# Performance work log

Measured on AMD Instinct MI355X. Metric: run time of the kernel, lower is better.

## Reference

```python
import jax, jax.numpy as jnp
import numpy as np

B, L, D = 1, 2048, 512
NL, N, K = 4, 16, 4
DI = 2 * D          # mamba expand=2
R = D // 16         # dt_rank = ceil(D/16)
H = 4 * D           # mlp hidden


def _ln(x, w, b, eps=1e-5):
    mu = x.mean(-1, keepdims=True)
    v = ((x - mu) ** 2).mean(-1, keepdims=True)
    return (x - mu) * jax.lax.rsqrt(v + eps) * w + b


def _rms(x, w, eps=1e-5):
    return x * jax.lax.rsqrt((x * x).mean(-1, keepdims=True) + eps) * w


def _ssm_scan(delta, Bm, Cm, u, A, Dp):
    # delta,u: (B,L,DI); Bm,Cm: (B,L,N); A: (DI,N); Dp: (DI,)
    def step(h, inp):
        d_t, b_t, c_t, u_t = inp                              # (B,DI),(B,N),(B,N),(B,DI)
        dA = jnp.exp(d_t[..., None] * A)                      # (B,DI,N)
        h = dA * h + (d_t * u_t)[..., None] * b_t[:, None, :]
        y = jnp.einsum('bdn,bn->bd', h, c_t)
        return h, y
    h0 = jnp.zeros((delta.shape[0], DI, N), delta.dtype)
    xs = (delta.swapaxes(0, 1), Bm.swapaxes(0, 1), Cm.swapaxes(0, 1), u.swapaxes(0, 1))
    _, ys = jax.lax.scan(step, h0, xs)
    return ys.swapaxes(0, 1) + u * Dp


def _mamba(h, in_w, cw, cb, xw, dtw, dtb, A_log, Dp, ow):
    xz = h @ in_w.T                                           # (B,L,2*DI)
    x, z = jnp.split(xz, 2, axis=-1)
    # causal depthwise conv1d, kernel K, left pad K-1
    xp = jnp.pad(x, ((0, 0), (K - 1, 0), (0, 0)))
    Ls = x.shape[1]
    x = sum(cw[:, k] * xp[:, k:k + Ls, :] for k in range(K)) + cb
    x = jax.nn.silu(x)
    dbc = x @ xw.T                                            # (B,L,R+2N)
    dt, Bm, Cm = dbc[..., :R], dbc[..., R:R + N], dbc[..., R + N:]
    delta = jax.nn.softplus(dt @ dtw.T + dtb)                 # (B,L,DI)
    A = -jnp.exp(A_log)                                       # (DI,N)
    y = _ssm_scan(delta, Bm, Cm, x, A, Dp)
    y = y * jax.nn.silu(z)
    return y @ ow.T


def _forward(hidden_states, ln1_w, ln1_b, in_proj_w, conv_w, conv_b, x_proj_w,
             dt_proj_w, dt_proj_b, A_log, D_param, out_proj_w, block_norm_w,
             norm_f_w, ln2_w, ln2_b, fc1_w, fc1_b, fc2_w, fc2_b):
    shortcut = hidden_states
    h = _ln(hidden_states, ln1_w, ln1_b)
    residual = None
    for i in range(in_proj_w.shape[0]):
        residual = h if residual is None else h + residual    # residual_in_fp32
        hn = _rms(residual, block_norm_w[i])                  # fused_add_norm prenorm
        h = _mamba(hn, in_proj_w[i], conv_w[i], conv_b[i], x_proj_w[i],
                   dt_proj_w[i], dt_proj_b[i], A_log[i], D_param[i], out_proj_w[i])
    h = _rms(h + residual, norm_f_w)                          # final rms_norm_fn
    h = shortcut + h
    x = _ln(h, ln2_w, ln2_b)
    x = jax.nn.gelu(x @ fc1_w.T + fc1_b)
    x = x @ fc2_w.T + fc2_b
    return h + x


def setup_inputs() -> dict:
    key = jax.random.key(0)
    ks = jax.random.split(key, 9)
    s = 0.02
    return {
        'hidden_states': jax.random.normal(ks[0], (B, L, D), jnp.float32),
        'ln1_w': jnp.ones((D,), jnp.float32),
        'ln1_b': jnp.zeros((D,), jnp.float32),
        'in_proj_w': jax.random.normal(ks[1], (NL, 2 * DI, D), jnp.float32) * s,
        'conv_w': jax.random.normal(ks[2], (NL, DI, K), jnp.float32) * 0.3,
        'conv_b': jnp.zeros((NL, DI), jnp.float32),
        'x_proj_w': jax.random.normal(ks[3], (NL, R + 2 * N, DI), jnp.float32) * s,
        'dt_proj_w': jax.random.normal(ks[4], (NL, DI, R), jnp.float32) * s,
        'dt_proj_b': jax.random.uniform(ks[5], (NL, DI), jnp.float32, -4.0, -2.0),
        'A_log': jnp.tile(jnp.log(jnp.arange(1, N + 1, dtype=jnp.float32)), (NL, DI, 1)),
        'D_param': jnp.ones((NL, DI), jnp.float32),
        'out_proj_w': jax.random.normal(ks[6], (NL, D, DI), jnp.float32) * s,
        'block_norm_w': jnp.ones((NL, D), jnp.float32),
        'norm_f_w': jnp.ones((D,), jnp.float32),
        'ln2_w': jnp.ones((D,), jnp.float32),
        'ln2_b': jnp.zeros((D,), jnp.float32),
        'fc1_w': jax.random.normal(ks[7], (H, D), jnp.float32) * s,
        'fc1_b': jnp.zeros((H,), jnp.float32),
        'fc2_w': jax.random.normal(ks[8], (D, H), jnp.float32) * s,
        'fc2_b': jnp.zeros((D,), jnp.float32),
    }


def reference(hidden_states, ln1_w, ln1_b, in_proj_w, conv_w, conv_b, x_proj_w,
              dt_proj_w, dt_proj_b, A_log, D_param, out_proj_w, block_norm_w,
              norm_f_w, ln2_w, ln2_b, fc1_w, fc1_b, fc2_w, fc2_b):
    return _forward(hidden_states, ln1_w, ln1_b, in_proj_w, conv_w, conv_b,
                    x_proj_w, dt_proj_w, dt_proj_b, A_log, D_param, out_proj_w,
                    block_norm_w, norm_f_w, ln2_w, ln2_b, fc1_w, fc1_b, fc2_w, fc2_b)
```

## Files before the change

kernel.cpp:

```cpp
#include <hip/hip_runtime.h>
#include <hip/hip_bf16.h>
#include <math.h>

#define L_SEQ 2048
#define Dm    512
#define DI    1024
#define Nst   16
#define Kc    4
#define Rr    32
#define NL    4
#define CH    128
#define LC    (L_SEQ / CH)
#define KSX   8

typedef __attribute__((ext_vector_type(8))) short bf16x8;
typedef __attribute__((ext_vector_type(4))) float f32x4;

__device__ __forceinline__ float act_softplus(float x) {
    return fmaxf(x, 0.f) + log1pf(__expf(-fabsf(x)));
}
__device__ __forceinline__ float act_gelu(float x) {
    float c = 0.7978845608028654f * (x + 0.044715f * x * x * x);
    float t = 1.f - 2.f / (__expf(2.f * c) + 1.f);
    return 0.5f * x * (1.f + t);
}
__device__ __forceinline__ float silu_(float x) {
    return x / (1.f + __expf(-x));
}
__device__ __forceinline__ ushort f2bf(float f) {
    union { float f; unsigned u; } c; c.f = f;
    unsigned r = c.u + 0x7fffu + ((c.u >> 16) & 1u);
    return (ushort)(r >> 16);
}
__device__ __forceinline__ float bf2f(ushort u) {
    union { unsigned u; float f; } c; c.u = ((unsigned)u) << 16;
    return c.f;
}
__device__ __forceinline__ float wave_sum(float v) {
    #pragma unroll
    for (int off = 32; off; off >>= 1) v += __shfl_xor(v, off);
    return v;
}

__global__ __launch_bounds__(256) void cast_all_kernel(
    const float* __restrict__ s0, ushort* __restrict__ d0, int n0,
    const float* __restrict__ s1, ushort* __restrict__ d1, int n1,
    const float* __restrict__ s2, ushort* __restrict__ d2, int n2,
    const float* __restrict__ s3, ushort* __restrict__ d3, int n3,
    const float* __restrict__ s4, ushort* __restrict__ d4, int n4_,
    const float* __restrict__ s5, ushort* __restrict__ d5, int n5)
{
    int i = blockIdx.x * 256 + threadIdx.x;
    const float* s; ushort* d;
    if (i < n0) { s = s0; d = d0; }
    else { i -= n0; if (i < n1) { s = s1; d = d1; }
    else { i -= n1; if (i < n2) { s = s2; d = d2; }
    else { i -= n2; if (i < n3) { s = s3; d = d3; }
    else { i -= n3; if (i < n4_) { s = s4; d = d4; }
    else { i -= n4_; if (i < n5) { s = s5; d = d5; } else return; } } } } }
    float4 v = ((const float4*)s)[i];
    ushort4 o;
    o.x = f2bf(v.x); o.y = f2bf(v.y); o.z = f2bf(v.z); o.w = f2bf(v.w);
    ((ushort4*)d)[i] = o;
}

__global__ __launch_bounds__(256) void ln_rms_kernel(const float* __restrict__ x,
    const float* __restrict__ w, const float* __restrict__ b,
    const float* __restrict__ rw, float* __restrict__ res,
    ushort* __restrict__ hn_bf)
{
    int lane = threadIdx.x & 63, wv = threadIdx.x >> 6;
    int row = blockIdx.x * 4 + wv;
    size_t base = (size_t)row * Dm + lane * 8;
    float v[8];
    *(float4*)(v)     = *(const float4*)(x + base);
    *(float4*)(v + 4) = *(const float4*)(x + base + 4);
    float s = 0.f, ss = 0.f;
    #pragma unroll
    for (int q = 0; q < 8; ++q) { s += v[q]; ss += v[q] * v[q]; }
    s = wave_sum(s); ss = wave_sum(ss);
    float mu = s * (1.f / Dm);
    float rs = rsqrtf(ss * (1.f / Dm) - mu * mu + 1e-5f);
    float wv8[8], bv8[8], rv8[8];
    *(float4*)(wv8)     = *(const float4*)(w + lane * 8);
    *(float4*)(wv8 + 4) = *(const float4*)(w + lane * 8 + 4);
    *(float4*)(bv8)     = *(const float4*)(b + lane * 8);
    *(float4*)(bv8 + 4) = *(const float4*)(b + lane * 8 + 4);
    *(float4*)(rv8)     = *(const float4*)(rw + lane * 8);
    *(float4*)(rv8 + 4) = *(const float4*)(rw + lane * 8 + 4);
    float o[8], ss2 = 0.f;
    #pragma unroll
    for (int q = 0; q < 8; ++q) {
        o[q] = (v[q] - mu) * rs * wv8[q] + bv8[q];
        ss2 += o[q] * o[q];
    }
    *(float4*)(res + base)     = *(float4*)(o);
    *(float4*)(res + base + 4) = *(float4*)(o + 4);
    ss2 = wave_sum(ss2);
    float rr = rsqrtf(ss2 * (1.f / Dm) + 1e-5f);
    bf16x8 hb;
    #pragma unroll
    for (int q = 0; q < 8; ++q) hb[q] = (short)f2bf(o[q] * rr * rv8[q]);
    *(bf16x8*)(hn_bf + base) = hb;
}

__global__ __launch_bounds__(256) void add_rms_kernel(const ushort* __restrict__ hb,
    float* __restrict__ res, const float* __restrict__ w, ushort* __restrict__ rms_out)
{
    int lane = threadIdx.x & 63, wv = threadIdx.x >> 6;
    int row = blockIdx.x * 4 + wv;
    size_t base = (size_t)row * Dm + lane * 8;
    bf16x8 hv = *(const bf16x8*)(hb + base);
    float v[8];
    *(float4*)(v)     = *(const float4*)(res + base);
    *(float4*)(v + 4) = *(const float4*)(res + base + 4);
    float ss = 0.f;
    #pragma unroll
    for (int q = 0; q < 8; ++q) {
        v[q] += bf2f((ushort)hv[q]);
        ss += v[q] * v[q];
    }
    *(float4*)(res + base)     = *(float4*)(v);
    *(float4*)(res + base + 4) = *(float4*)(v + 4);
    ss = wave_sum(ss);
    float rr = rsqrtf(ss * (1.f / Dm) + 1e-5f);
    float wv8[8];
    *(float4*)(wv8)     = *(const float4*)(w + lane * 8);
    *(float4*)(wv8 + 4) = *(const float4*)(w + lane * 8 + 4);
    bf16x8 ob;
    #pragma unroll
    for (int q = 0; q < 8; ++q) ob[q] = (short)f2bf(v[q] * rr * wv8[q]);
    *(bf16x8*)(rms_out + base) = ob;
}

__global__ __launch_bounds__(256) void final_ln2_kernel(const ushort* __restrict__ hb,
    const float* __restrict__ res, const float* __restrict__ shortcut,
    const float* __restrict__ wf, const float* __restrict__ w2,
    const float* __restrict__ b2, float* __restrict__ hout,
    ushort* __restrict__ yb16)
{
    int lane = threadIdx.x & 63, wv = threadIdx.x >> 6;
    int row = blockIdx.x * 4 + wv;
    size_t base = (size_t)row * Dm + lane * 8;
    bf16x8 hv = *(const bf16x8*)(hb + base);
    float v[8];
    *(float4*)(v)     = *(const float4*)(res + base);
    *(float4*)(v + 4) = *(const float4*)(res + base + 4);
    float ss = 0.f;
    #pragma unroll
    for (int q = 0; q < 8; ++q) {
        v[q] += bf2f((ushort)hv[q]);
        ss += v[q] * v[q];
    }
    ss = wave_sum(ss);
    float rs = rsqrtf(ss * (1.f / Dm) + 1e-5f);
    float sc[8], wf8[8];
    *(float4*)(sc)     = *(const float4*)(shortcut + base);
    *(float4*)(sc + 4) = *(const float4*)(shortcut + base + 4);
    *(float4*)(wf8)     = *(const float4*)(wf + lane * 8);
    *(float4*)(wf8 + 4) = *(const float4*)(wf + lane * 8 + 4);
    float t[8], s2 = 0.f, ss2 = 0.f;
    #pragma unroll
    for (int q = 0; q < 8; ++q) {
        t[q] = sc[q] + v[q] * rs * wf8[q];
        s2 += t[q]; ss2 += t[q] * t[q];
    }
    *(float4*)(hout + base)     = *(float4*)(t);
    *(float4*)(hout + base + 4) = *(float4*)(t + 4);
    s2 = wave_sum(s2); ss2 = wave_sum(ss2);
    float mu = s2 * (1.f / Dm);
    float rsig = rsqrtf(ss2 * (1.f / Dm) - mu * mu + 1e-5f);
    float w28[8], b28[8];
    *(float4*)(w28)     = *(const float4*)(w2 + lane * 8);
    *(float4*)(w28 + 4) = *(const float4*)(w2 + lane * 8 + 4);
    *(float4*)(b28)     = *(const float4*)(b2 + lane * 8);
    *(float4*)(b28 + 4) = *(const float4*)(b2 + lane * 8 + 4);
    bf16x8 ob;
    #pragma unroll
    for (int q = 0; q < 8; ++q) ob[q] = (short)f2bf((t[q] - mu) * rsig * w28[q] + b28[q]);
    *(bf16x8*)(yb16 + base) = ob;
}

template<int BM, int BN, int BK, int EPI, int KS = 1>
__global__ __launch_bounds__(256) void gemm_mfma(
    const ushort* __restrict__ A, int lda,
    const ushort* __restrict__ W, int K,
    void* __restrict__ Cout, int ldc,
    const float* __restrict__ bias, const float* __restrict__ addsrc,
    size_t split_stride)
{
    constexpr int ROWB  = BK * 2;
    constexpr int SMASK = (ROWB / 16) - 1;
    constexpr int KK    = BK / 32;
    constexpr int WM = BM / 2, WN = BN / 2;
    constexpr int FM = WM / 16, FN = WN / 16;
    constexpr int ISS_A = (BM * ROWB) / 4096;
    constexpr int ISS_W = (BN * ROWB) / 4096;

    __shared__ __align__(16) ushort As[BM * BK];
    __shared__ __align__(16) ushort Ws[BN * BK];

    int tid = threadIdx.x;
    int wave = tid >> 6, lane = tid & 63;
    int wr = wave >> 1, wc = wave & 1;
    int l16 = lane & 15, lk = lane >> 4;
    int bm = blockIdx.y * BM, bn = blockIdx.x * BN;

    int kbeg = 0, kend = K;
    float* coutf = (float*)Cout;
    if constexpr (KS > 1) {
        int Kper = K / KS;
        kbeg = blockIdx.z * Kper; kend = kbeg + Kper;
        coutf += split_stride * blockIdx.z;
    }

    const ushort* srcA[ISS_A];
    const ushort* srcW[ISS_W];
    #pragma unroll
    for (int s = 0; s < ISS_A; ++s) {
        int off = s * 4096 + wave * 1024 + lane * 16;
        int row = off / ROWB;
        int slot = (off % ROWB) >> 4;
        int col = ((slot ^ (row & SMASK)) << 3);
        srcA[s] = A + (size_t)(bm + row) * lda + col;
    }
    #pragma unroll
    for (int s = 0; s < ISS_W; ++s) {
        int off = s * 4096 + wave * 1024 + lane * 16;
        int row = off / ROWB;
        int slot = (off % ROWB) >> 4;
        int col = ((slot ^ (row & SMASK)) << 3);
        srcW[s] = W + (size_t)(bn + row) * K + col;
    }
    int aoff[FM][KK], woff[FN][KK];
    #pragma unroll
    for (int i = 0; i < FM; ++i) {
        int row = wr * WM + i * 16 + l16;
        #pragma unroll
        for (int kk = 0; kk < KK; ++kk)
            aoff[i][kk] = row * BK + ((((kk << 2) | lk) ^ (row & SMASK)) << 3);
    }
    #pragma unroll
    for (int j = 0; j < FN; ++j) {
        int row = wc * WN + j * 16 + l16;
        #pragma unroll
        for (int kk = 0; kk < KK; ++kk)
            woff[j][kk] = row * BK + ((((kk << 2) | lk) ^ (row & SMASK)) << 3);
    }

    f32x4 acc[FM][FN] = {};

    for (int k0 = kbeg; k0 < kend; k0 += BK) {
        #pragma unroll
        for (int s = 0; s < ISS_A; ++s)
            __builtin_amdgcn_global_load_lds(
                (const __attribute__((address_space(1))) void*)(srcA[s] + k0),
                (__attribute__((address_space(3))) void*)((char*)As + s * 4096 + wave * 1024),
                16, 0, 0);
        #pragma unroll
        for (int s = 0; s < ISS_W; ++s)
            __builtin_amdgcn_global_load_lds(
                (const __attribute__((address_space(1))) void*)(srcW[s] + k0),
                (__attribute__((address_space(3))) void*)((char*)Ws + s * 4096 + wave * 1024),
                16, 0, 0);
        __syncthreads();
        #pragma unroll
        for (int kk = 0; kk < KK; ++kk) {
            bf16x8 af[FM], wf[FN];
            #pragma unroll
            for (int i = 0; i < FM; ++i) af[i] = *(const bf16x8*)(As + aoff[i][kk]);
            #pragma unroll
            for (int j = 0; j < FN; ++j) wf[j] = *(const bf16x8*)(Ws + woff[j][kk]);
            #pragma unroll
            for (int i = 0; i < FM; ++i)
                #pragma unroll
                for (int j = 0; j < FN; ++j)
                    acc[i][j] = __builtin_amdgcn_mfma_f32_16x16x32_bf16(af[i], wf[j], acc[i][j], 0, 0, 0);
        }
        __syncthreads();
    }

    int orow0 = bm + wr * WM, ocol0 = bn + wc * WN;
    #pragma unroll
    for (int j = 0; j < FN; ++j) {
        int col = ocol0 + j * 16 + l16;
        float bj = 0.f;
        if constexpr (EPI == 2 || EPI == 4) bj = bias[col];
        #pragma unroll
        for (int i = 0; i < FM; ++i) {
            #pragma unroll
            for (int r = 0; r < 4; ++r) {
                int row = orow0 + i * 16 + lk * 4 + r;
                float v = acc[i][j][r];
                if constexpr (EPI == 0) {
                    coutf[(size_t)row * ldc + col] = v;
                } else if constexpr (EPI == 1) {
                    ((ushort*)Cout)[(size_t)row * ldc + col] = f2bf(v);
                } else if constexpr (EPI == 2) {
                    ((ushort*)Cout)[(size_t)row * ldc + col] = f2bf(act_gelu(v + bj));
                } else if constexpr (EPI == 4) {
                    ((float*)Cout)[(size_t)row * ldc + col] = v + bj + addsrc[(size_t)row * ldc + col];
                }
            }
        }
    }
}

__global__ __launch_bounds__(256) void conv_silu_kernel(const ushort* __restrict__ xz,
    const float* __restrict__ cw, const float* __restrict__ cb, ushort* __restrict__ xc)
{
    int g = blockIdx.x * 256 + threadIdx.x;
    int e = g * 8;
    int d0 = e & (DI - 1);
    int t = e >> 10;
    float acc[8];
    #pragma unroll
    for (int q = 0; q < 8; ++q) acc[q] = cb[d0 + q];
    float4 cwv[8];
    #pragma unroll
    for (int q = 0; q < 8; ++q) cwv[q] = *(const float4*)(cw + (size_t)(d0 + q) * 4);
    #pragma unroll
    for (int k = 0; k < 4; ++k) {
        int tt = t + k - 3;
        if (tt >= 0) {
            bf16x8 xv = *(const bf16x8*)(xz + (size_t)tt * (2 * DI) + d0);
            #pragma unroll
            for (int q = 0; q < 8; ++q) {
                float wk = (k == 0) ? cwv[q].x : (k == 1) ? cwv[q].y : (k == 2) ? cwv[q].z : cwv[q].w;
                acc[q] = fmaf(wk, bf2f((ushort)xv[q]), acc[q]);
            }
        }
    }
    bf16x8 o;
    #pragma unroll
    for (int q = 0; q < 8; ++q) o[q] = (short)f2bf(silu_(acc[q]));
    *(bf16x8*)(xc + e) = o;
}

__global__ __launch_bounds__(256) void scan_chunk_kernel(
    const float* __restrict__ part, const ushort* __restrict__ u,
    const ushort* __restrict__ wdt, const float* __restrict__ dtb,
    const float* __restrict__ A_log,
    float* __restrict__ hend, float* __restrict__ aprod,
    ushort* __restrict__ delta_bf)
{
    __shared__ float sdt[LC][32];
    __shared__ float bsm[LC][16];
    int tid = threadIdx.x;
    int c = blockIdx.x;
    int d = blockIdx.y * 256 + tid;
    int t0 = c * LC;
    const int S = L_SEQ * 64;
    for (int i = tid; i < LC * 48; i += 256) {
        int tt = i / 48, cc = i % 48;
        int idx = (t0 + tt) * 64 + cc;
        float s = 0.f;
        #pragma unroll
        for (int p = 0; p < KSX; ++p) s += part[idx + p * S];
        if (cc < 32) sdt[tt][cc] = s; else bsm[tt][cc - 32] = s;
    }
    bf16x8 wd[4];
    #pragma unroll
    for (int p = 0; p < 4; ++p) wd[p] = *(const bf16x8*)(wdt + (size_t)d * 32 + p * 8);
    float bd = dtb[d];
    float A2[16];
    {
        float a[16];
        #pragma unroll
        for (int q = 0; q < 4; ++q)
            *(float4*)(a + q * 4) = ((const float4*)(A_log + (size_t)d * 16))[q];
        #pragma unroll
        for (int n = 0; n < 16; ++n)
            A2[n] = -__expf(a[n]) * 1.44269504f;
    }
    float h[16], ap[16];
    #pragma unroll
    for (int n = 0; n < 16; ++n) { h[n] = 0.f; ap[n] = 1.f; }
    __syncthreads();
    for (int tt = 0; tt < LC; ++tt) {
        int t = t0 + tt;
        float dtv = bd;
        #pragma unroll
        for (int p = 0; p < 4; ++p)
            #pragma unroll
            for (int e = 0; e < 8; ++e)
                dtv = fmaf(sdt[tt][p * 8 + e], bf2f((ushort)wd[p][e]), dtv);
        ushort dbf = f2bf(act_softplus(dtv));
        delta_bf[(size_t)t * DI + d] = dbf;
        float dt_ = bf2f(dbf);
        float du = dt_ * bf2f(u[(size_t)t * DI + d]);
        #pragma unroll
        for (int n = 0; n < 16; ++n) {
            float dA = exp2f(dt_ * A2[n]);
            h[n] = fmaf(dA, h[n], du * bsm[tt][n]);
            ap[n] *= dA;
        }
    }
    size_t base = ((size_t)c * DI + d) * 16;
    #pragma unroll
    for (int q = 0; q < 4; ++q) {
        ((float4*)(hend + base))[q]  = *(float4*)(h + q * 4);
        ((float4*)(aprod + base))[q] = *(float4*)(ap + q * 4);
    }
}

__global__ __launch_bounds__(64) void chunk_prefix_kernel(
    const float* __restrict__ hend, float* __restrict__ aprod_hin)
{
    int j = blockIdx.x * 64 + threadIdx.x;
    float h = 0.f;
    for (int cg = 0; cg < CH; cg += 8) {
        float ap[8], he[8];
        #pragma unroll
        for (int q = 0; q < 8; ++q) {
            size_t o = (size_t)(cg + q) * (DI * Nst) + j;
            ap[q] = aprod_hin[o]; he[q] = hend[o];
        }
        #pragma unroll
        for (int q = 0; q < 8; ++q) {
            size_t o = (size_t)(cg + q) * (DI * Nst) + j;
            aprod_hin[o] = h;
            h = fmaf(ap[q], h, he[q]);
        }
    }
}

__global__ __launch_bounds__(256) void scan_apply_kernel(
    const float* __restrict__ part, const ushort* __restrict__ delta,
    const ushort* __restrict__ u, const float* __restrict__ A_log,
    const float* __restrict__ Dp, const ushort* __restrict__ xz,
    const float* __restrict__ hin, ushort* __restrict__ y)
{
    __shared__ float bsm[LC][16], csm[LC][16];
    int tid = threadIdx.x;
    int c = blockIdx.x;
    int d = blockIdx.y * 256 + tid;
    int t0 = c * LC;
    const int S = L_SEQ * 64;
    for (int i = tid; i < LC * 32; i += 256) {
        int tt = i >> 5, k = i & 31;
        int idx = (t0 + tt) * 64 + 32 + k;
        float s = 0.f;
        #pragma unroll
        for (int p = 0; p < KSX; ++p) s += part[idx + p * S];
        if (k < 16) bsm[tt][k] = s; else csm[tt][k - 16] = s;
    }
    float A2[16];
    {
        float a[16];
        #pragma unroll
        for (int q = 0; q < 4; ++q)
            *(float4*)(a + q * 4) = ((const float4*)(A_log + (size_t)d * 16))[q];
        #pragma unroll
        for (int n = 0; n < 16; ++n)
            A2[n] = -__expf(a[n]) * 1.44269504f;
    }
    float h[16];
    size_t base = ((size_t)c * DI + d) * 16;
    #pragma unroll
    for (int q = 0; q < 4; ++q)
        *(float4*)(h + q * 4) = ((const float4*)(hin + base))[q];
    float Dval = Dp[d];
    __syncthreads();
    for (int tt = 0; tt < LC; ++tt) {
        int t = t0 + tt;
        float dt_ = bf2f(delta[(size_t)t * DI + d]);
        float u_  = bf2f(u[(size_t)t * DI + d]);
        float du  = dt_ * u_;
        float acc = 0.f;
        #pragma unroll
        for (int n = 0; n < 16; ++n) {
            float dA = exp2f(dt_ * A2[n]);
            h[n] = fmaf(dA, h[n], du * bsm[tt][n]);
            acc = fmaf(h[n], csm[tt][n], acc);
        }
        float zv = bf2f(xz[(size_t)t * (2 * DI) + DI + d]);
        y[(size_t)t * DI + d] = f2bf((acc + u_ * Dval) * silu_(zv));
    }
}

extern "C" void kernel_launch(void* const* d_in, const int* in_sizes, int n_in,
                              void* d_out, int out_size, void* d_ws, size_t ws_size,
                              hipStream_t stream)
{
    const float* hidden     = (const float*)d_in[0];
    const float* ln1_w      = (const float*)d_in[1];
    const float* ln1_b      = (const float*)d_in[2];
    const float* in_proj_w  = (const float*)d_in[3];
    const float* conv_w     = (const float*)d_in[4];
    const float* conv_b     = (const float*)d_in[5];
    const float* x_proj_w   = (const float*)d_in[6];
    const float* dt_proj_w  = (const float*)d_in[7];
    const float* dt_proj_b  = (const float*)d_in[8];
    const float* A_log      = (const float*)d_in[9];
    const float* D_param    = (const float*)d_in[10];
    const float* out_proj_w = (const float*)d_in[11];
    const float* block_norm_w = (const float*)d_in[12];
    const float* norm_f_w   = (const float*)d_in[13];
    const float* ln2_w      = (const float*)d_in[14];
    const float* ln2_b      = (const float*)d_in[15];
    const float* fc1_w      = (const float*)d_in[16];
    const float* fc1_b      = (const float*)d_in[17];
    const float* fc2_w      = (const float*)d_in[18];
    const float* fc2_b      = (const float*)d_in[19];

    char* P = (char*)d_ws;
    auto alloc = [&](size_t bytes) { char* r = P; P += (bytes + 255) & ~(size_t)255; return r; };
    float* hout   = (float*)alloc((size_t)L_SEQ * Dm * 4);
    float* res    = (float*)alloc((size_t)L_SEQ * Dm * 4);
    float* part   = (float*)alloc((size_t)KSX * L_SEQ * 64 * 4);
    float* hend   = (float*)alloc((size_t)CH * DI * Nst * 4);
    float* aprod  = (float*)alloc((size_t)CH * DI * Nst * 4);
    ushort* h_bf  = (ushort*)alloc((size_t)L_SEQ * Dm * 2);
    ushort* delta_bf = (ushort*)alloc((size_t)L_SEQ * DI * 2);
    ushort* hn_bf = (ushort*)alloc((size_t)L_SEQ * Dm * 2);
    ushort* xz_bf = (ushort*)alloc((size_t)L_SEQ * 2 * DI * 2);
    ushort* xc_bf = (ushort*)alloc((size_t)L_SEQ * DI * 2);
    ushort* yb_bf = (ushort*)alloc((size_t)L_SEQ * DI * 2);
    ushort* w_in  = (ushort*)alloc((size_t)NL * 2 * DI * Dm * 2);
    ushort* w_out = (ushort*)alloc((size_t)NL * Dm * DI * 2);
    ushort* w_x   = (ushort*)alloc((size_t)NL * 64 * DI * 2);
    ushort* w_dt  = (ushort*)alloc((size_t)NL * DI * Rr * 2);
    ushort* w_fc1 = (ushort*)alloc((size_t)(4 * Dm) * Dm * 2);
    ushort* w_fc2 = (ushort*)alloc((size_t)Dm * (4 * Dm) * 2);
    float* out  = (float*)d_out;

    {
        int n0 = NL * 2 * DI * Dm / 4, n1 = NL * Dm * DI / 4, n2 = NL * 64 * DI / 4;
        int n3 = NL * DI * Rr / 4, n4_ = 4 * Dm * Dm / 4, n5 = Dm * 4 * Dm / 4;
        int tot = n0 + n1 + n2 + n3 + n4_ + n5;
        cast_all_kernel<<<(tot + 255) / 256, 256, 0, stream>>>(
            in_proj_w, w_in, n0, out_proj_w, w_out, n1, x_proj_w, w_x, n2,
            dt_proj_w, w_dt, n3, fc1_w, w_fc1, n4_, fc2_w, w_fc2, n5);
    }

    ln_rms_kernel<<<L_SEQ / 4, 256, 0, stream>>>(hidden, ln1_w, ln1_b,
                                                 block_norm_w, res, hn_bf);

    dim3 gscan(CH, DI / 256);
    for (int i = 0; i < NL; ++i) {
        if (i) add_rms_kernel<<<L_SEQ / 4, 256, 0, stream>>>(h_bf, res,
                                                  block_norm_w + i * Dm, hn_bf);
        gemm_mfma<128, 128, 128, 1><<<dim3(2 * DI / 128, L_SEQ / 128), 256, 0, stream>>>(
            hn_bf, Dm, w_in + (size_t)i * 2 * DI * Dm, Dm, xz_bf, 2 * DI, nullptr, nullptr, 0);
        conv_silu_kernel<<<(L_SEQ * DI / 8) / 256, 256, 0, stream>>>(
            xz_bf, conv_w + i * DI * Kc, conv_b + i * DI, xc_bf);
        gemm_mfma<64, 64, 64, 0, KSX><<<dim3(1, L_SEQ / 64, KSX), 256, 0, stream>>>(
            xc_bf, DI, w_x + (size_t)i * 64 * DI, DI, part, 64, nullptr, nullptr,
            (size_t)L_SEQ * 64);
        scan_chunk_kernel<<<gscan, 256, 0, stream>>>(part, xc_bf,
                                        w_dt + (size_t)i * DI * Rr, dt_proj_b + i * DI,
                                        A_log + (size_t)i * DI * Nst, hend, aprod, delta_bf);
        chunk_prefix_kernel<<<(DI * Nst) / 64, 64, 0, stream>>>(hend, aprod);
        scan_apply_kernel<<<gscan, 256, 0, stream>>>(part, delta_bf, xc_bf,
                                        A_log + (size_t)i * DI * Nst,
                                        D_param + i * DI, xz_bf, aprod, yb_bf);
        gemm_mfma<64, 64, 128, 1><<<dim3(Dm / 64, L_SEQ / 64), 256, 0, stream>>>(
            yb_bf, DI, w_out + (size_t)i * Dm * DI, DI, h_bf, Dm, nullptr, nullptr, 0);
    }

    final_ln2_kernel<<<L_SEQ / 4, 256, 0, stream>>>(h_bf, res, hidden, norm_f_w,
                                                ln2_w, ln2_b, hout, hn_bf);
    gemm_mfma<128, 128, 128, 2><<<dim3(2048 / 128, L_SEQ / 128), 256, 0, stream>>>(
        hn_bf, Dm, w_fc1, Dm, xz_bf, 2048, fc1_b, nullptr, 0);
    gemm_mfma<64, 64, 128, 4><<<dim3(Dm / 64, L_SEQ / 64), 256, 0, stream>>>(
        xz_bf, 2048, w_fc2, 2048, out, Dm, fc2_b, hout, 0);
}
```

Before: 429.5 us.

## Fuse chunked scan phases into one persistent kernel with grid barriers

Merges scan_chunk, chunk_prefix and scan_apply into a single 512-block kernel that synchronises through a hierarchical atomic grid barrier (8 groups of 64 blocks). The delta intermediate is no longer stored; dt is recomputed from shared memory in the second pass. The prefix phase now runs on 64 blocks of 256 threads instead of 256 blocks of 64. The initial LayerNorm/RMS kernel is folded into the weight-cast kernel, which also zeroes the barrier counters. This removes two launches per layer and the delta round trip. In exchange it adds barrier spin cost and depends on all 512 blocks being co-resident, with launch_bounds(256,2) as the occupancy hint.

Result: slower. 1.681 ms (+291.5%).

```diff
diff --git a/kernel.cpp b/kernel.cpp
--- a/kernel.cpp
+++ b/kernel.cpp
@@ -42,15 +42,82 @@
     return v;
 }
 
-__global__ __launch_bounds__(256) void cast_all_kernel(
+__device__ __forceinline__ void hbar(unsigned* base, int g, int grpSize, int nGrps) {
+    __syncthreads();
+    __threadfence();
+    if (threadIdx.x == 0) {
+        unsigned* grp  = base + g * 16;
+        unsigned* glob = base + 8 * 16;
+        unsigned* rel  = base + (9 + g) * 16;
+        unsigned prev = __hip_atomic_fetch_add(grp, 1u, __ATOMIC_ACQ_REL, __HIP_MEMORY_SCOPE_AGENT);
+        if (prev == (unsigned)(grpSize - 1)) {
+            __hip_atomic_fetch_add(glob, 1u, __ATOMIC_ACQ_REL, __HIP_MEMORY_SCOPE_AGENT);
+            while (__hip_atomic_load(glob, __ATOMIC_ACQUIRE, __HIP_MEMORY_SCOPE_AGENT) < (unsigned)nGrps)
+                __builtin_amdgcn_s_sleep(2);
+            __hip_atomic_store(rel, 1u, __ATOMIC_RELEASE, __HIP_MEMORY_SCOPE_AGENT);
+        } else {
+            while (__hip_atomic_load(rel, __ATOMIC_ACQUIRE, __HIP_MEMORY_SCOPE_AGENT) == 0u)
+                __builtin_amdgcn_s_sleep(2);
+        }
+    }
+    __syncthreads();
+    __threadfence();
+}
+
+__global__ __launch_bounds__(256) void setup_kernel(
     const float* __restrict__ s0, ushort* __restrict__ d0, int n0,
     const float* __restrict__ s1, ushort* __restrict__ d1, int n1,
     const float* __restrict__ s2, ushort* __restrict__ d2, int n2,
     const float* __restrict__ s3, ushort* __restrict__ d3, int n3,
     const float* __restrict__ s4, ushort* __restrict__ d4, int n4_,
-    const float* __restrict__ s5, ushort* __restrict__ d5, int n5)
-{
-    int i = blockIdx.x * 256 + threadIdx.x;
+    const float* __restrict__ s5, ushort* __restrict__ d5, int n5,
+    const float* __restrict__ x, const float* __restrict__ w,
+    const float* __restrict__ b, const float* __restrict__ rw,
+    float* __restrict__ res, ushort* __restrict__ hn_bf,
+    unsigned* __restrict__ ctr)
+{
+    if (blockIdx.x < 512) {
+        int lane = threadIdx.x & 63, wv = threadIdx.x >> 6;
+        int row = blockIdx.x * 4 + wv;
+        size_t base = (size_t)row * Dm + lane * 8;
+        float v[8];
+        *(float4*)(v)     = *(const float4*)(x + base);
+        *(float4*)(v + 4) = *(const float4*)(x + base + 4);
+        float s = 0.f, ss = 0.f;
+        #pragma unroll
+        for (int q = 0; q < 8; ++q) { s += v[q]; ss += v[q] * v[q]; }
+        s = wave_sum(s); ss = wave_sum(ss);
+        float mu = s * (1.f / Dm);
+        float rs = rsqrtf(ss * (1.f / Dm) - mu * mu + 1e-5f);
+        float wv8[8], bv8[8], rv8[8];
+        *(float4*)(wv8)     = *(const float4*)(w + lane * 8);
+        *(float4*)(wv8 + 4) = *(const float4*)(w + lane * 8 + 4);
+        *(float4*)(bv8)     = *(const float4*)(b + lane * 8);
+        *(float4*)(bv8 + 4) = *(const float4*)(b + lane * 8 + 4);
+        *(float4*)(rv8)     = *(const float4*)(rw + lane * 8);
+        *(float4*)(rv8 + 4) = *(const float4*)(rw + lane * 8 + 4);
+        float o[8], ss2 = 0.f;
+        #pragma unroll
+        for (int q = 0; q < 8; ++q) {
+            o[q] = (v[q] - mu) * rs * wv8[q] + bv8[q];
+            ss2 += o[q] * o[q];
+        }
+        *(float4*)(res + base)     = *(float4*)(o);
+        *(float4*)(res + base + 4) = *(float4*)(o + 4);
+        ss2 = wave_sum(ss2);
+        float rr = rsqrtf(ss2 * (1.f / Dm) + 1e-5f);
+        bf16x8 hb;
+        #pragma unroll
+        for (int q = 0; q < 8; ++q) hb[q] = (short)f2bf(o[q] * rr * rv8[q]);
+        *(bf16x8*)(hn_bf + base) = hb;
+        return;
+    }
+    int cb = blockIdx.x - 512;
+    if (cb == 0) {
+        #pragma unroll
+        for (int q = 0; q < 16; ++q) ctr[threadIdx.x * 16 + q] = 0u;
+    }
+    int i = cb * 256 + threadIdx.x;
     const float* s; ushort* d;
     if (i < n0) { s = s0; d = d0; }
     else { i -= n0; if (i < n1) { s = s1; d = d1; }
@@ -62,46 +129,6 @@
     ushort4 o;
     o.x = f2bf(v.x); o.y = f2bf(v.y); o.z = f2bf(v.z); o.w = f2bf(v.w);
     ((ushort4*)d)[i] = o;
-}
-
-__global__ __launch_bounds__(256) void ln_rms_kernel(const float* __restrict__ x,
-    const float* __restrict__ w, const float* __restrict__ b,
-    const float* __restrict__ rw, float* __restrict__ res,
-    ushort* __restrict__ hn_bf)
-{
-    int lane = threadIdx.x & 63, wv = threadIdx.x >> 6;
-    int row = blockIdx.x * 4 + wv;
-    size_t base = (size_t)row * Dm + lane * 8;
-    float v[8];
-    *(float4*)(v)     = *(const float4*)(x + base);
-    *(float4*)(v + 4) = *(const float4*)(x + base + 4);
-    float s = 0.f, ss = 0.f;
-    #pragma unroll
-    for (int q = 0; q < 8; ++q) { s += v[q]; ss += v[q] * v[q]; }
-    s = wave_sum(s); ss = wave_sum(ss);
-    float mu = s * (1.f / Dm);
-    float rs = rsqrtf(ss * (1.f / Dm) - mu * mu + 1e-5f);
-    float wv8[8], bv8[8], rv8[8];
-    *(float4*)(wv8)     = *(const float4*)(w + lane * 8);
-    *(float4*)(wv8 + 4) = *(const float4*)(w + lane * 8 + 4);
-    *(float4*)(bv8)     = *(const float4*)(b + lane * 8);
-    *(float4*)(bv8 + 4) = *(const float4*)(b + lane * 8 + 4);
-    *(float4*)(rv8)     = *(const float4*)(rw + lane * 8);
-    *(float4*)(rv8 + 4) = *(const float4*)(rw + lane * 8 + 4);
-    float o[8], ss2 = 0.f;
-    #pragma unroll
-    for (int q = 0; q < 8; ++q) {
-        o[q] = (v[q] - mu) * rs * wv8[q] + bv8[q];
-        ss2 += o[q] * o[q];
-    }
-    *(float4*)(res + base)     = *(float4*)(o);
-    *(float4*)(res + base + 4) = *(float4*)(o + 4);
-    ss2 = wave_sum(ss2);
-    float rr = rsqrtf(ss2 * (1.f / Dm) + 1e-5f);
-    bf16x8 hb;
-    #pragma unroll
-    for (int q = 0; q < 8; ++q) hb[q] = (short)f2bf(o[q] * rr * rv8[q]);
-    *(bf16x8*)(hn_bf + base) = hb;
 }
 
 __global__ __launch_bounds__(256) void add_rms_kernel(const ushort* __restrict__ hb,
@@ -337,27 +364,35 @@
     *(bf16x8*)(xc + e) = o;
 }
 
-__global__ __launch_bounds__(256) void scan_chunk_kernel(
+__global__ __launch_bounds__(256, 2) void scan_fused_kernel(
     const float* __restrict__ part, const ushort* __restrict__ u,
     const ushort* __restrict__ wdt, const float* __restrict__ dtb,
-    const float* __restrict__ A_log,
+    const float* __restrict__ A_log, const float* __restrict__ Dp,
+    const ushort* __restrict__ xz,
     float* __restrict__ hend, float* __restrict__ aprod,
-    ushort* __restrict__ delta_bf)
+    ushort* __restrict__ y, unsigned* __restrict__ ctr)
 {
     __shared__ float sdt[LC][32];
     __shared__ float bsm[LC][16];
+    __shared__ float csm[LC][16];
     int tid = threadIdx.x;
-    int c = blockIdx.x;
-    int d = blockIdx.y * 256 + tid;
+    int bid = blockIdx.x;
+    int c = bid & (CH - 1);
+    int yg = bid >> 7;
+    int d = yg * 256 + tid;
+    int g = bid & 7;
     int t0 = c * LC;
     const int S = L_SEQ * 64;
-    for (int i = tid; i < LC * 48; i += 256) {
-        int tt = i / 48, cc = i % 48;
+
+    for (int i = tid; i < LC * 64; i += 256) {
+        int tt = i >> 6, cc = i & 63;
         int idx = (t0 + tt) * 64 + cc;
         float s = 0.f;
         #pragma unroll
         for (int p = 0; p < KSX; ++p) s += part[idx + p * S];
-        if (cc < 32) sdt[tt][cc] = s; else bsm[tt][cc - 32] = s;
+        if (cc < 32) sdt[tt][cc] = s;
+        else if (cc < 48) bsm[tt][cc - 32] = s;
+        else csm[tt][cc - 48] = s;
     }
     bf16x8 wd[4];
     #pragma unroll
@@ -377,6 +412,7 @@
     #pragma unroll
     for (int n = 0; n < 16; ++n) { h[n] = 0.f; ap[n] = 1.f; }
     __syncthreads();
+
     for (int tt = 0; tt < LC; ++tt) {
         int t = t0 + tt;
         float dtv = bd;
@@ -385,92 +421,64 @@
             #pragma unroll
             for (int e = 0; e < 8; ++e)
                 dtv = fmaf(sdt[tt][p * 8 + e], bf2f((ushort)wd[p][e]), dtv);
-        ushort dbf = f2bf(act_softplus(dtv));
-        delta_bf[(size_t)t * DI + d] = dbf;
-        float dt_ = bf2f(dbf);
-        float du = dt_ * bf2f(u[(size_t)t * DI + d]);
+        dtv = act_softplus(dtv);
+        float du = dtv * bf2f(u[(size_t)t * DI + d]);
         #pragma unroll
         for (int n = 0; n < 16; ++n) {
-            float dA = exp2f(dt_ * A2[n]);
+            float dA = exp2f(dtv * A2[n]);
             h[n] = fmaf(dA, h[n], du * bsm[tt][n]);
             ap[n] *= dA;
         }
     }
-    size_t base = ((size_t)c * DI + d) * 16;
+    size_t sbase = ((size_t)c * DI + d) * 16;
     #pragma unroll
     for (int q = 0; q < 4; ++q) {
-        ((float4*)(hend + base))[q]  = *(float4*)(h + q * 4);
-        ((float4*)(aprod + base))[q] = *(float4*)(ap + q * 4);
-    }
-}
-
-__global__ __launch_bounds__(64) void chunk_prefix_kernel(
-    const float* __restrict__ hend, float* __restrict__ aprod_hin)
-{
-    int j = blockIdx.x * 64 + threadIdx.x;
-    float h = 0.f;
-    for (int cg = 0; cg < CH; cg += 8) {
-        float ap[8], he[8];
-        #pragma unroll
-        for (int q = 0; q < 8; ++q) {
-            size_t o = (size_t)(cg + q) * (DI * Nst) + j;
-            ap[q] = aprod_hin[o]; he[q] = hend[o];
-        }
-        #pragma unroll
-        for (int q = 0; q < 8; ++q) {
-            size_t o = (size_t)(cg + q) * (DI * Nst) + j;
-            aprod_hin[o] = h;
-            h = fmaf(ap[q], h, he[q]);
-        }
-    }
-}
-
-__global__ __launch_bounds__(256) void scan_apply_kernel(
-    const float* __restrict__ part, const ushort* __restrict__ delta,
-    const ushort* __restrict__ u, const float* __restrict__ A_log,
-    const float* __restrict__ Dp, const ushort* __restrict__ xz,
-    const float* __restrict__ hin, ushort* __restrict__ y)
-{
-    __shared__ float bsm[LC][16], csm[LC][16];
-    int tid = threadIdx.x;
-    int c = blockIdx.x;
-    int d = blockIdx.y * 256 + tid;
-    int t0 = c * LC;
-    const int S = L_SEQ * 64;
-    for (int i = tid; i < LC * 32; i += 256) {
-        int tt = i >> 5, k = i & 31;
-        int idx = (t0 + tt) * 64 + 32 + k;
-        float s = 0.f;
-        #pragma unroll
-        for (int p = 0; p < KSX; ++p) s += part[idx + p * S];
-        if (k < 16) bsm[tt][k] = s; else csm[tt][k - 16] = s;
-    }
-    float A2[16];
-    {
-        float a[16];
-        #pragma unroll
-        for (int q = 0; q < 4; ++q)
-            *(float4*)(a + q * 4) = ((const float4*)(A_log + (size_t)d * 16))[q];
-        #pragma unroll
-        for (int n = 0; n < 16; ++n)
-            A2[n] = -__expf(a[n]) * 1.44269504f;
-    }
-    float h[16];
-    size_t base = ((size_t)c * DI + d) * 16;
+        ((float4*)(hend + sbase))[q]  = *(float4*)(h + q * 4);
+        ((float4*)(aprod + sbase))[q] = *(float4*)(ap + q * 4);
+    }
+
+    hbar(ctr, g, 64, 8);
+
+    if (bid < 64) {
+        int j = bid * 256 + tid;
+        float hh = 0.f;
+        for (int cg = 0; cg < CH; cg += 8) {
+            float apv[8], hev[8];
+            #pragma unroll
+            for (int q = 0; q < 8; ++q) {
+                size_t o = (size_t)(cg + q) * (DI * Nst) + j;
+                apv[q] = aprod[o]; hev[q] = hend[o];
+            }
+            #pragma unroll
+            for (int q = 0; q < 8; ++q) {
+                size_t o = (size_t)(cg + q) * (DI * Nst) + j;
+                aprod[o] = hh;
+                hh = fmaf(apv[q], hh, hev[q]);
+            }
+        }
+    }
+
+    hbar(ctr + 512, g, 64, 8);
+
     #pragma unroll
     for (int q = 0; q < 4; ++q)
-        *(float4*)(h + q * 4) = ((const float4*)(hin + base))[q];
+        *(float4*)(h + q * 4) = ((const float4*)(aprod + sbase))[q];
     float Dval = Dp[d];
-    __syncthreads();
     for (int tt = 0; tt < LC; ++tt) {
         int t = t0 + tt;
-        float dt_ = bf2f(delta[(size_t)t * DI + d]);
-        float u_  = bf2f(u[(size_t)t * DI + d]);
-        float du  = dt_ * u_;
+        float dtv = bd;
+        #pragma unroll
+        for (int p = 0; p < 4; ++p)
+            #pragma unroll
+            for (int e = 0; e < 8; ++e)
+                dtv = fmaf(sdt[tt][p * 8 + e], bf2f((ushort)wd[p][e]), dtv);
+        dtv = act_softplus(dtv);
+        float u_ = bf2f(u[(size_t)t * DI + d]);
+        float du = dtv * u_;
         float acc = 0.f;
         #pragma unroll
         for (int n = 0; n < 16; ++n) {
-            float dA = exp2f(dt_ * A2[n]);
+            float dA = exp2f(dtv * A2[n]);
             h[n] = fmaf(dA, h[n], du * bsm[tt][n]);
             acc = fmaf(h[n], csm[tt][n], acc);
         }
@@ -511,8 +519,8 @@
     float* part   = (float*)alloc((size_t)KSX * L_SEQ * 64 * 4);
     float* hend   = (float*)alloc((size_t)CH * DI * Nst * 4);
     float* aprod  = (float*)alloc((size_t)CH * DI * Nst * 4);
+    unsigned* ctr = (unsigned*)alloc((size_t)NL * 1024 * 4);
     ushort* h_bf  = (ushort*)alloc((size_t)L_SEQ * Dm * 2);
-    ushort* delta_bf = (ushort*)alloc((size_t)L_SEQ * DI * 2);
     ushort* hn_bf = (ushort*)alloc((size_t)L_SEQ * Dm * 2);
     ushort* xz_bf = (ushort*)alloc((size_t)L_SEQ * 2 * DI * 2);
     ushort* xc_bf = (ushort*)alloc((size_t)L_SEQ * DI * 2);
@@ -529,15 +537,13 @@
         int n0 = NL * 2 * DI * Dm / 4, n1 = NL * Dm * DI / 4, n2 = NL * 64 * DI / 4;
         int n3 = NL * DI * Rr / 4, n4_ = 4 * Dm * Dm / 4, n5 = Dm * 4 * Dm / 4;
         int tot = n0 + n1 + n2 + n3 + n4_ + n5;
-        cast_all_kernel<<<(tot + 255) / 256, 256, 0, stream>>>(
+        int grid = 512 + (tot + 255) / 256;
+        setup_kernel<<<grid, 256, 0, stream>>>(
             in_proj_w, w_in, n0, out_proj_w, w_out, n1, x_proj_w, w_x, n2,
-            dt_proj_w, w_dt, n3, fc1_w, w_fc1, n4_, fc2_w, w_fc2, n5);
-    }
-
-    ln_rms_kernel<<<L_SEQ / 4, 256, 0, stream>>>(hidden, ln1_w, ln1_b,
-                                                 block_norm_w, res, hn_bf);
-
-    dim3 gscan(CH, DI / 256);
+            dt_proj_w, w_dt, n3, fc1_w, w_fc1, n4_, fc2_w, w_fc2, n5,
+            hidden, ln1_w, ln1_b, block_norm_w, res, hn_bf, ctr);
+    }
+
     for (int i = 0; i < NL; ++i) {
         if (i) add_rms_kernel<<<L_SEQ / 4, 256, 0, stream>>>(h_bf, res,
                                                   block_norm_w + i * Dm, hn_bf);
@@ -548,13 +554,10 @@
         gemm_mfma<64, 64, 64, 0, KSX><<<dim3(1, L_SEQ / 64, KSX), 256, 0, stream>>>(
             xc_bf, DI, w_x + (size_t)i * 64 * DI, DI, part, 64, nullptr, nullptr,
             (size_t)L_SEQ * 64);
-        scan_chunk_kernel<<<gscan, 256, 0, stream>>>(part, xc_bf,
+        scan_fused_kernel<<<512, 256, 0, stream>>>(part, xc_bf,
                                         w_dt + (size_t)i * DI * Rr, dt_proj_b + i * DI,
-                                        A_log + (size_t)i * DI * Nst, hend, aprod, delta_bf);
-        chunk_prefix_kernel<<<(DI * Nst) / 64, 64, 0, stream>>>(hend, aprod);
-        scan_apply_kernel<<<gscan, 256, 0, stream>>>(part, delta_bf, xc_bf,
-                                        A_log + (size_t)i * DI * Nst,
-                                        D_param + i * DI, xz_bf, aprod, yb_bf);
+                                        A_log + (size_t)i * DI * Nst, D_param + i * DI,
+                                        xz_bf, hend, aprod, yb_bf, ctr + (size_t)i * 1024);
         gemm_mfma<64, 64, 128, 1><<<dim3(Dm / 64, L_SEQ / 64), 256, 0, stream>>>(
             yb_bf, DI, w_out + (size_t)i * Dm * DI, DI, h_bf, Dm, nullptr, nullptr, 0);
     }
```
